# Performance work log

Hardware: AMD Instinct MI355X
Metric: run time of the kernel (lower is better)

## Reference

```python
import jax, jax.numpy as jnp
import numpy as np

B, C_IN, C_OUT, H, W, S = 8, 32, 32, 128, 128, 1024


def setup_inputs() -> dict:
    key = jax.random.key(0)
    k1, k2, k3 = jax.random.split(key, 3)
    v = jax.random.normal(k1, (B, C_IN, H, W), dtype=jnp.float32)
    # kaiming-normal-ish init for weight (O, I, 2): std = sqrt(2 / fan_in)
    fan_in = C_IN * 2
    weight = jax.random.normal(k2, (C_OUT, C_IN, 2), dtype=jnp.float32) * np.sqrt(2.0 / fan_in)
    # randperm(J)[:S] -> sample without replacement
    indices = jax.random.permutation(k3, H * W)[:S].astype(jnp.int64)
    return {"v": v, "weight": weight, "indices": indices}


def reference(v, weight, indices):
    b, c_in, h, w = v.shape
    c_out = weight.shape[0]
    J = h * w
    # meshgrid with indexing='xy': grids have shape (h, w)
    xs = jnp.linspace(-1.0, 1.0, w, dtype=v.dtype)
    ys = jnp.linspace(-1.0, 1.0, h, dtype=v.dtype)
    xg, yg = jnp.meshgrid(xs, ys, indexing="xy")          # (h, w) each
    coords = jnp.stack((xg, yg), axis=-1).reshape(J, 2)    # (J, 2)
    vp = v.transpose(0, 2, 3, 1).reshape(b, J, c_in)       # (B, J, Cin)
    sample_coords = coords[indices]                        # (S, 2)
    sample_vp = vp[:, indices]                             # (B, S, Cin)
    # Faithful math: u[b,o,r] = sum_{s,i,c} W[o,i,c] * (coords[r,c]-sample_coords[s,c]) * sv[b,s,i]
    # Fused: contract sampled values with weight first (small bsoc), then with diff.
    A = jnp.einsum("bsi,oic->bsoc", sample_vp, weight)     # (B, S, O, 2)
    diff = coords[:, None, :] - sample_coords[None, :, :]  # (J, S, 2)
    u = jnp.einsum("rsc,bsoc->bor", diff, A)               # (B, O, J)
    return u.reshape(b, c_out, h, w)
```

## Files before the change

kernel.cpp:

```cpp
#include <hip/hip_runtime.h>
#include <hip/hip_bf16.h>

#define BDIM 8
#define CIN 32
#define COUT 32
#define HDIM 128
#define WDIM 128
#define JDIM (HDIM * WDIM)
#define SDIM 1024
#define PARTS 16
#define SPP (SDIM / PARTS)

#define PARTIALS_FLOATS (PARTS * BDIM * 96)

__global__ __launch_bounds__(256) void k_gather(const float* __restrict__ v,
                                                const int* __restrict__ idx,
                                                float* __restrict__ partials) {
    const int b    = blockIdx.x / PARTS;
    const int part = blockIdx.x % PARTS;
    const int i    = threadIdx.x & 31;
    const int sg   = threadIdx.x >> 5;

    const float* vb = v + ((size_t)(b * CIN + i)) * JDIM;

    float p = 0.f, q0 = 0.f, q1 = 0.f;
    const float step = 2.0f / 127.0f;

    const int s0 = part * SPP;
#pragma unroll 4
    for (int s = s0 + sg; s < s0 + SPP; s += 8) {
        const int j = idx[s];
        const int x = j & (WDIM - 1);
        const int y = j >> 7;
        const float scx = -1.0f + (float)x * step;
        const float scy = -1.0f + (float)y * step;
        const float val = vb[j];
        p  += val;
        q0 += val * scx;
        q1 += val * scy;
    }

    __shared__ float red[8][96];
    red[sg][i * 3 + 0] = p;
    red[sg][i * 3 + 1] = q0;
    red[sg][i * 3 + 2] = q1;
    __syncthreads();

    if (threadIdx.x < 96) {
        float sum = 0.f;
#pragma unroll
        for (int g = 0; g < 8; ++g) sum += red[g][threadIdx.x];
        partials[((size_t)part * BDIM + b) * 96 + threadIdx.x] = sum;
    }
}

__global__ __launch_bounds__(256) void k_tk(const float* __restrict__ partials,
                                            const float* __restrict__ w,
                                            float* __restrict__ tk) {
    __shared__ float pq[BDIM][96];

    for (int slot = threadIdx.x; slot < BDIM * 96; slot += 256) {
        float s = 0.f;
#pragma unroll
        for (int part = 0; part < PARTS; ++part)
            s += partials[(size_t)part * BDIM * 96 + slot];
        pq[slot / 96][slot % 96] = s;
    }
    __syncthreads();

    const int b = threadIdx.x >> 5;
    const int o = threadIdx.x & 31;

    float t0 = 0.f, t1 = 0.f, k = 0.f;
#pragma unroll
    for (int i = 0; i < CIN; ++i) {
        const float P  = pq[b][i * 3 + 0];
        const float Q0 = pq[b][i * 3 + 1];
        const float Q1 = pq[b][i * 3 + 2];
        const float w0 = w[(o * CIN + i) * 2 + 0];
        const float w1 = w[(o * CIN + i) * 2 + 1];
        t0 += P * w0;
        t1 += P * w1;
        k  += Q0 * w0 + Q1 * w1;
    }
    tk[threadIdx.x]       = t0;
    tk[256 + threadIdx.x] = t1;
    tk[512 + threadIdx.x] = -(t0 + t1 + k);
}

__global__ __launch_bounds__(256) void k_out(const float* __restrict__ tk,
                                             float* __restrict__ out) {
    const int bo      = blockIdx.x >> 2;
    const int quarter = blockIdx.x & 3;

    const float T0 = tk[bo];
    const float T1 = tk[256 + bo];
    const float C0 = tk[512 + bo];
    const float a  = T0 * (2.0f / 127.0f);
    const float c  = T1 * (2.0f / 127.0f);

    float* outp = out + (size_t)bo * JDIM;
    const int r0 = quarter * (JDIM / 4);

#pragma unroll
    for (int seg = 0; seg < 4; ++seg) {
        const int r = r0 + (seg * 256 + threadIdx.x) * 4;
        const int x = r & (WDIM - 1);
        const int y = r >> 7;
        const float base = (float)y * c + C0;
        float4 val;
        val.x = base + (float)(x + 0) * a;
        val.y = base + (float)(x + 1) * a;
        val.z = base + (float)(x + 2) * a;
        val.w = base + (float)(x + 3) * a;
        *reinterpret_cast<float4*>(outp + r) = val;
    }
}

extern "C" void kernel_launch(void* const* d_in, const int* in_sizes, int n_in,
                              void* d_out, int out_size, void* d_ws, size_t ws_size,
                              hipStream_t stream) {
    const float* v   = (const float*)d_in[0];
    const float* w   = (const float*)d_in[1];
    const int*   idx = (const int*)d_in[2];
    float* out = (float*)d_out;

    float* partials = (float*)d_ws;
    float* tk       = partials + PARTIALS_FLOATS;

    k_gather<<<BDIM * PARTS, 256, 0, stream>>>(v, idx, partials);
    k_tk<<<1, 256, 0, stream>>>(partials, w, tk);
    k_out<<<1024, 256, 0, stream>>>(tk, out);
}
```

Baseline: 83.35 us.

## Fuse weight-contraction kernel into output kernel and widen gather parallelism

Removes the single-block k_tk launch by having each output block reduce the gather partials for its batch and contract them with its output channel's weights using wave shuffles, then write the affine plane. The gather kernel doubles its partition count and fully unrolls four independent index loads per thread to expose more memory-level parallelism. This saves a kernel launch and a serial dependency, at the cost of 1024 blocks each redundantly summing 32 partials and doing a small reduction before streaming output.

New measurement: 77.37 us. -7.2%, faster.

```diff
diff --git a/kernel.cpp b/kernel.cpp
--- a/kernel.cpp
+++ b/kernel.cpp
@@ -8,36 +8,41 @@
 #define WDIM 128
 #define JDIM (HDIM * WDIM)
 #define SDIM 1024
-#define PARTS 16
+#define PARTS 32
 #define SPP (SDIM / PARTS)
 
-#define PARTIALS_FLOATS (PARTS * BDIM * 96)
 
 __global__ __launch_bounds__(256) void k_gather(const float* __restrict__ v,
                                                 const int* __restrict__ idx,
                                                 float* __restrict__ partials) {
-    const int b    = blockIdx.x / PARTS;
-    const int part = blockIdx.x % PARTS;
+    const int b    = blockIdx.x >> 5;
+    const int part = blockIdx.x & (PARTS - 1);
     const int i    = threadIdx.x & 31;
     const int sg   = threadIdx.x >> 5;
 
     const float* vb = v + ((size_t)(b * CIN + i)) * JDIM;
-
-    float p = 0.f, q0 = 0.f, q1 = 0.f;
     const float step = 2.0f / 127.0f;
 
-    const int s0 = part * SPP;
-#pragma unroll 4
-    for (int s = s0 + sg; s < s0 + SPP; s += 8) {
-        const int j = idx[s];
-        const int x = j & (WDIM - 1);
-        const int y = j >> 7;
-        const float scx = -1.0f + (float)x * step;
-        const float scy = -1.0f + (float)y * step;
-        const float val = vb[j];
-        p  += val;
-        q0 += val * scx;
-        q1 += val * scy;
+    const int s0 = part * SPP + sg;
+    int j0 = idx[s0 + 0];
+    int j1 = idx[s0 + 8];
+    int j2 = idx[s0 + 16];
+    int j3 = idx[s0 + 24];
+    float v0 = vb[j0], v1 = vb[j1], v2 = vb[j2], v3 = vb[j3];
+
+    float p = v0 + v1 + v2 + v3;
+    float q0 = 0.f, q1 = 0.f;
+    {
+        const float x0 = -1.0f + (float)(j0 & (WDIM - 1)) * step;
+        const float y0 = -1.0f + (float)(j0 >> 7) * step;
+        const float x1 = -1.0f + (float)(j1 & (WDIM - 1)) * step;
+        const float y1 = -1.0f + (float)(j1 >> 7) * step;
+        const float x2 = -1.0f + (float)(j2 & (WDIM - 1)) * step;
+        const float y2 = -1.0f + (float)(j2 >> 7) * step;
+        const float x3 = -1.0f + (float)(j3 & (WDIM - 1)) * step;
+        const float y3 = -1.0f + (float)(j3 >> 7) * step;
+        q0 = v0 * x0 + v1 * x1 + v2 * x2 + v3 * x3;
+        q1 = v0 * y0 + v1 * y1 + v2 * y2 + v3 * y3;
     }
 
     __shared__ float red[8][96];
@@ -54,50 +59,54 @@
     }
 }
 
-__global__ __launch_bounds__(256) void k_tk(const float* __restrict__ partials,
-                                            const float* __restrict__ w,
-                                            float* __restrict__ tk) {
-    __shared__ float pq[BDIM][96];
+__global__ __launch_bounds__(256) void k_out(const float* __restrict__ partials,
+                                             const float* __restrict__ w,
+                                             float* __restrict__ out) {
+    const int bo      = blockIdx.x >> 2;
+    const int quarter = blockIdx.x & 3;
+    const int b       = bo >> 5;
+    const int o       = bo & 31;
 
-    for (int slot = threadIdx.x; slot < BDIM * 96; slot += 256) {
+    __shared__ float pq[96];
+    __shared__ float coef[3];
+
+    if (threadIdx.x < 96) {
         float s = 0.f;
 #pragma unroll
         for (int part = 0; part < PARTS; ++part)
-            s += partials[(size_t)part * BDIM * 96 + slot];
-        pq[slot / 96][slot % 96] = s;
+            s += partials[((size_t)part * BDIM + b) * 96 + threadIdx.x];
+        pq[threadIdx.x] = s;
     }
     __syncthreads();
 
-    const int b = threadIdx.x >> 5;
-    const int o = threadIdx.x & 31;
-
-    float t0 = 0.f, t1 = 0.f, k = 0.f;
-#pragma unroll
-    for (int i = 0; i < CIN; ++i) {
-        const float P  = pq[b][i * 3 + 0];
-        const float Q0 = pq[b][i * 3 + 1];
-        const float Q1 = pq[b][i * 3 + 2];
+    if (threadIdx.x < 64) {
+        const int i = threadIdx.x & 31;
+        const float P  = pq[i * 3 + 0];
+        const float Q0 = pq[i * 3 + 1];
+        const float Q1 = pq[i * 3 + 2];
         const float w0 = w[(o * CIN + i) * 2 + 0];
         const float w1 = w[(o * CIN + i) * 2 + 1];
-        t0 += P * w0;
-        t1 += P * w1;
-        k  += Q0 * w0 + Q1 * w1;
+        float t0 = P * w0;
+        float t1 = P * w1;
+        float kk = Q0 * w0 + Q1 * w1;
+#pragma unroll
+        for (int off = 16; off >= 1; off >>= 1) {
+            t0 += __shfl_xor(t0, off);
+            t1 += __shfl_xor(t1, off);
+            kk += __shfl_xor(kk, off);
+        }
+        if (threadIdx.x == 0) {
+            const float step = 2.0f / 127.0f;
+            coef[0] = t0 * step;
+            coef[1] = t1 * step;
+            coef[2] = -(t0 + t1 + kk);
+        }
     }
-    tk[threadIdx.x]       = t0;
-    tk[256 + threadIdx.x] = t1;
-    tk[512 + threadIdx.x] = -(t0 + t1 + k);
-}
+    __syncthreads();
 
-__global__ __launch_bounds__(256) void k_out(const float* __restrict__ tk,
-                                             float* __restrict__ out) {
-    const int bo      = blockIdx.x >> 2;
-    const int quarter = blockIdx.x & 3;
-
-    const float T0 = tk[bo];
-    const float T1 = tk[256 + bo];
-    const float C0 = tk[512 + bo];
-    const float a  = T0 * (2.0f / 127.0f);
-    const float c  = T1 * (2.0f / 127.0f);
+    const float a  = coef[0];
+    const float c  = coef[1];
+    const float C0 = coef[2];
 
     float* outp = out + (size_t)bo * JDIM;
     const int r0 = quarter * (JDIM / 4);
@@ -126,9 +135,7 @@
     float* out = (float*)d_out;
 
     float* partials = (float*)d_ws;
-    float* tk       = partials + PARTIALS_FLOATS;
 
     k_gather<<<BDIM * PARTS, 256, 0, stream>>>(v, idx, partials);
-    k_tk<<<1, 256, 0, stream>>>(partials, w, tk);
-    k_out<<<1024, 256, 0, stream>>>(tk, out);
+    k_out<<<1024, 256, 0, stream>>>(partials, w, out);
 }
```
